# Kernel tuning notes

Hardware: AMD Instinct MI355X
Metric: run time of the kernel (lower is better)

The kernel has to match this reference:

```python
import jax, jax.numpy as jnp
import numpy as np

N_NODES = 100000
N_EDGES = 1600000
IN_DIM, HIDDEN_DIM, OUT_DIM = 500, 64, 40


def setup_inputs() -> dict:
    key = jax.random.key(0)
    k1, k2, k3, k4, k5 = jax.random.split(key, 5)
    x = jax.random.normal(k1, (N_NODES, IN_DIM), dtype=jnp.float32)
    edge_index = jax.random.randint(k2, (2, N_EDGES), 0, N_NODES, dtype=jnp.int64)
    # Glorot-style init like PyG GCNConv
    W1 = jax.random.normal(k3, (IN_DIM, HIDDEN_DIM), dtype=jnp.float32) / np.sqrt(IN_DIM)
    b1 = jnp.zeros((HIDDEN_DIM,), dtype=jnp.float32)
    W2 = jax.random.normal(k4, (HIDDEN_DIM, OUT_DIM), dtype=jnp.float32) / np.sqrt(HIDDEN_DIM)
    b2 = jnp.zeros((OUT_DIM,), dtype=jnp.float32)
    return {"x": x, "W1": W1, "b1": b1, "W2": W2, "b2": b2, "edge_index": edge_index}


def _gcn_conv(x, W, b, src, dst, n):
    """PyG GCNConv: h = D^{-1/2} (A + I) D^{-1/2} (x W) + b."""
    h = x @ W  # transform first, propagate in smaller dim
    loops = jnp.arange(n, dtype=src.dtype)
    s = jnp.concatenate([src, loops])
    d = jnp.concatenate([dst, loops])
    deg = jax.ops.segment_sum(jnp.ones_like(d, dtype=h.dtype), d, num_segments=n)
    dinv = jnp.where(deg > 0, jax.lax.rsqrt(deg), 0.0)
    norm = dinv[s] * dinv[d]               # [E+N]
    msg = h[s] * norm[:, None]             # gather + scale
    out = jax.ops.segment_sum(msg, d, num_segments=n)  # scatter-add
    return out + b


def reference(x, W1, b1, W2, b2, edge_index):
    src, dst = edge_index[0], edge_index[1]
    n = x.shape[0]
    h = _gcn_conv(x, W1, b1, src, dst, n)
    h = jax.nn.relu(h)  # eval mode: dropout is identity
    out = _gcn_conv(h, W2, b2, src, dst, n)
    return out
```

## Files before the change

### kernel.cpp

```cpp
#include <hip/hip_runtime.h>
#include <cstdint>
#include <cstddef>

#define NN 100000
#define NE 1600000
#define IND 500
#define HD 64
#define OD 40
#define NBLK ((NN + 255) / 256)
#define KSTEPS 16
#define NTT 16
#define EB 1563

typedef __attribute__((ext_vector_type(8))) short short8v;
typedef __attribute__((ext_vector_type(8))) __bf16 bf16x8;
typedef __attribute__((ext_vector_type(4))) float float4v;

template <class V>
static __device__ __forceinline__ auto mfma_bf16_(V a, V b, float4v c, int)
    -> decltype(__builtin_amdgcn_mfma_f32_16x16x32_bf16(a, b, c, 0, 0, 0)) {
    return __builtin_amdgcn_mfma_f32_16x16x32_bf16(a, b, c, 0, 0, 0);
}
template <class V>
static __device__ __forceinline__ float4v mfma_bf16_(V a, V b, float4v c, long) {
    return __builtin_amdgcn_mfma_f32_16x16x32_bf16((bf16x8)a, (bf16x8)b, c, 0, 0, 0);
}
static __device__ __forceinline__ float4v mfma16(short8v a, short8v b, float4v c) {
    return mfma_bf16_(a, b, c, 0);
}

static __device__ __forceinline__ float bf2f(unsigned short v) {
    return __uint_as_float((unsigned)v << 16);
}
static __device__ __forceinline__ unsigned short f2bf(float v) {
    unsigned u = __float_as_uint(v);
    return (unsigned short)((u + 0x7fffu + ((u >> 16) & 1u)) >> 16);
}

typedef __attribute__((address_space(3))) char lds_char;
typedef const __attribute__((address_space(1))) char g_char;
static __device__ __forceinline__ void gl16(const char* g, char* l) {
    __builtin_amdgcn_global_load_lds((g_char*)g, (lds_char*)l, 16, 0, 0);
}

static __device__ __forceinline__ int detect64(const void* ei) {
    const unsigned* u = (const unsigned*)ei;
    int is64 = 1;
    #pragma unroll
    for (int i = 1; i < 16; i += 2)
        if (u[i] != 0u) is64 = 0;
    return is64;
}

static __device__ __forceinline__ void load4e(const void* ei, int is64, size_t base, int v[4]) {
    if (is64) {
        int4 a = ((const int4*)ei)[base >> 1];
        int4 b = ((const int4*)ei)[(base >> 1) + 1];
        v[0] = a.x; v[1] = a.z; v[2] = b.x; v[3] = b.z;
    } else {
        int4 a = *(const int4*)((const int*)ei + base);
        v[0] = a.x; v[1] = a.y; v[2] = a.z; v[3] = a.w;
    }
}

__global__ __launch_bounds__(256) void k_count_prep(const void* ei, int* cnt,
                                                    int* __restrict__ rank,
                                                    const float* __restrict__ W,
                                                    unsigned short* __restrict__ wh,
                                                    unsigned short* __restrict__ wl) {
    const int is64 = detect64(ei);
    int e0 = (blockIdx.x * 256 + threadIdx.x) * 4;
    if (e0 < NE) {
        int d[4];
        load4e(ei, is64, (size_t)NE + e0, d);
        int4 r;
        r.x = atomicAdd(&cnt[d[0]], 1);
        r.y = atomicAdd(&cnt[d[1]], 1);
        r.z = atomicAdd(&cnt[d[2]], 1);
        r.w = atomicAdd(&cnt[d[3]], 1);
        *(int4*)(rank + e0) = r;
    }
    int t = blockIdx.x * 256 + threadIdx.x;
    if (t < KSTEPS * 4 * 64) {
        int l = t & 63;
        int f = (t >> 6) & 3;
        int s = t >> 8;
        int n = f * 16 + (l & 15);
        int kbase = s * 32 + 8 * (l >> 4);
        unsigned short* ph = wh + (size_t)t * 8;
        unsigned short* pl = wl + (size_t)t * 8;
        #pragma unroll
        for (int j = 0; j < 8; ++j) {
            int k = kbase + j;
            float v = (k < IND) ? W[(size_t)k * HD + n] : 0.f;
            unsigned u = __float_as_uint(v);
            ph[j] = (unsigned short)(u >> 16);
            float r = v - __uint_as_float(u & 0xffff0000u);
            pl[j] = f2bf(r);
        }
    }
}

__global__ __launch_bounds__(256) void k_scan_block(const int* __restrict__ cnt,
                                                    int* __restrict__ rowptr,
                                                    int* __restrict__ bsum,
                                                    float* __restrict__ dinv) {
    int t = threadIdx.x;
    int i = blockIdx.x * 256 + t;
    int v = (i < NN) ? cnt[i] : 0;
    if (i < NN) dinv[i] = rsqrtf((float)v + 1.0f);
    int inc = v;
    #pragma unroll
    for (int off = 1; off < 64; off <<= 1) {
        int u = __shfl_up(inc, off);
        if ((t & 63) >= off) inc += u;
    }
    __shared__ int wsum[4];
    if ((t & 63) == 63) wsum[t >> 6] = inc;
    __syncthreads();
    if (t == 0) {
        int a = 0;
        #pragma unroll
        for (int w = 0; w < 4; ++w) { int b = wsum[w]; wsum[w] = a; a += b; }
        bsum[blockIdx.x] = a;
    }
    __syncthreads();
    if (i < NN) rowptr[i] = inc - v + wsum[t >> 6];
}

__global__ __launch_bounds__(512) void k_scan_bsum(int* bsum) {
    int t = threadIdx.x;
    int v = (t < NBLK) ? bsum[t] : 0;
    int inc = v;
    #pragma unroll
    for (int off = 1; off < 64; off <<= 1) {
        int u = __shfl_up(inc, off);
        if ((t & 63) >= off) inc += u;
    }
    __shared__ int wsum[8];
    if ((t & 63) == 63) wsum[t >> 6] = inc;
    __syncthreads();
    if (t == 0) {
        int a = 0;
        #pragma unroll
        for (int w = 0; w < 8; ++w) { int b = wsum[w]; wsum[w] = a; a += b; }
    }
    __syncthreads();
    if (t < NBLK) bsum[t] = inc - v + wsum[t >> 6];
}

__global__ void k_scan_add(int* rowptr, const int* __restrict__ bsum) {
    int i = blockIdx.x * 256 + threadIdx.x;
    if (i < NN) rowptr[i] += bsum[i >> 8];
    if (i == 0) rowptr[NN] = NE;
}

static __device__ __forceinline__ void split8f(float4 u0, float4 u1,
                                               short8v& hi, short8v& lo) {
    float t[8] = {u0.x, u0.y, u0.z, u0.w, u1.x, u1.y, u1.z, u1.w};
    #pragma unroll
    for (int j = 0; j < 8; ++j) {
        unsigned q = __float_as_uint(t[j]);
        hi[j] = (short)(q >> 16);
        float r = t[j] - __uint_as_float(q & 0xffff0000u);
        lo[j] = (short)f2bf(r);
    }
}

__global__ __launch_bounds__(256, 5) void k_gemm_scatter(const float* __restrict__ x,
                                                         const char* __restrict__ whb,
                                                         const char* __restrict__ wlb,
                                                         const float* __restrict__ dinv,
                                                         unsigned short* __restrict__ h,
                                                         const void* __restrict__ ei,
                                                         const int* __restrict__ rowptr,
                                                         const int* __restrict__ rank,
                                                         int* __restrict__ srcs) {
    __shared__ char smem[32768];
    if (blockIdx.x & 1) {
        int e0 = ((blockIdx.x >> 1) * 256 + threadIdx.x) * 4;
        if (e0 >= NE) return;
        const int is64 = detect64(ei);
        int s[4], d[4];
        load4e(ei, is64, (size_t)e0, s);
        load4e(ei, is64, (size_t)NE + e0, d);
        int4 r = *(const int4*)(rank + e0);
        srcs[rowptr[d[0]] + r.x] = s[0];
        srcs[rowptr[d[1]] + r.y] = s[1];
        srcs[rowptr[d[2]] + r.z] = s[2];
        srcs[rowptr[d[3]] + r.w] = s[3];
        return;
    }
    const int tid  = threadIdx.x;
    const int lane = tid & 63;
    const int wave = tid >> 6;
    const int row0 = (blockIdx.x >> 1) * 64;
    const int rA = lane & 15;
    const int cg = lane >> 4;

    auto stage = [&](int kt, int buf) {
        const bool tail = (kt == NTT - 1);
        #pragma unroll
        for (int i = 0; i < 2; ++i) {
            int slot = i * 256 + tid;
            int r = slot >> 3, c = slot & 7;
            int cs = c ^ (r & 7);
            if (tail && cs > 4) cs = 4;
            int rsrc = row0 + r; if (rsrc >= NN) rsrc = NN - 1;
            const char* g = (const char*)x + (size_t)rsrc * (IND * 4) + kt * 128 + cs * 16;
            char* l = smem + buf * 16384 + (i * 256 + wave * 64) * 16;
            gl16(g, l);
        }
        #pragma unroll
        for (int i = 0; i < 2; ++i) {
            int j = i * 256 + tid;
            const char* src = (j < 256 ? whb : wlb) + kt * 4096 + (size_t)(j & 255) * 16;
            char* l = smem + buf * 16384 + 8192 + (i * 256 + wave * 64) * 16;
            gl16(src, l);
        }
    };

    float4v acc[4];
    const float4v zero4 = {0.f, 0.f, 0.f, 0.f};
    #pragma unroll
    for (int f = 0; f < 4; ++f) acc[f] = zero4;

    stage(0, 0);
    __syncthreads();

    int cur = 0;
    const int rbase = (wave * 16 + rA) * 8;
    const int sw = rA & 7;

    for (int kt = 0; kt < NTT; ++kt) {
        if (kt + 1 < NTT) stage(kt + 1, cur ^ 1);
        const float4*  pa = (const float4*)(smem + cur * 16384);
        const short8v* pb = (const short8v*)(smem + cur * 16384 + 8192);
        int ch = cg * 2;
        float4 u0 = pa[rbase + (ch ^ sw)];
        float4 u1 = pa[rbase + ((ch + 1) ^ sw)];
        short8v ah, al;
        split8f(u0, u1, ah, al);
        #pragma unroll
        for (int f = 0; f < 4; ++f) {
            short8v vh = pb[f * 64 + lane];
            short8v vl = pb[256 + f * 64 + lane];
            acc[f] = mfma16(al, vh, acc[f]);
            acc[f] = mfma16(ah, vl, acc[f]);
            acc[f] = mfma16(ah, vh, acc[f]);
        }
        __syncthreads();
        cur ^= 1;
    }

    #pragma unroll
    for (int j = 0; j < 4; ++j) {
        int row = row0 + wave * 16 + cg * 4 + j;
        if (row < NN) {
            float dv = dinv[row];
            #pragma unroll
            for (int f = 0; f < 4; ++f)
                h[(size_t)row * HD + f * 16 + rA] = f2bf(acc[f][j] * dv);
        }
    }
}

__global__ __launch_bounds__(256) void k_agg1(const int* __restrict__ rowptr,
                                              const int* __restrict__ srcs,
                                              const float* __restrict__ dinv,
                                              const unsigned short* __restrict__ hb,
                                              const float* __restrict__ bias,
                                              unsigned short* __restrict__ outb) {
    int wid = (blockIdx.x * 256 + threadIdx.x) >> 6;
    int lane = threadIdx.x & 63;
    if (wid >= NN) return;
    float acc = bf2f(hb[(size_t)wid * HD + lane]);
    int beg = rowptr[wid];
    int cnt = rowptr[wid + 1] - beg;
    for (int base = 0; base < cnt; base += 64) {
        int m = cnt - base; if (m > 64) m = 64;
        int sj = (lane < m) ? srcs[beg + base + lane] : 0;
        int j = 0;
        for (; j + 8 <= m; j += 8) {
            int s0 = __builtin_amdgcn_readlane(sj, j);
            int s1 = __builtin_amdgcn_readlane(sj, j + 1);
            int s2 = __builtin_amdgcn_readlane(sj, j + 2);
            int s3 = __builtin_amdgcn_readlane(sj, j + 3);
            int s4 = __builtin_amdgcn_readlane(sj, j + 4);
            int s5 = __builtin_amdgcn_readlane(sj, j + 5);
            int s6 = __builtin_amdgcn_readlane(sj, j + 6);
            int s7 = __builtin_amdgcn_readlane(sj, j + 7);
            float v0 = bf2f(hb[(size_t)s0 * HD + lane]);
            float v1 = bf2f(hb[(size_t)s1 * HD + lane]);
            float v2 = bf2f(hb[(size_t)s2 * HD + lane]);
            float v3 = bf2f(hb[(size_t)s3 * HD + lane]);
            float v4 = bf2f(hb[(size_t)s4 * HD + lane]);
            float v5 = bf2f(hb[(size_t)s5 * HD + lane]);
            float v6 = bf2f(hb[(size_t)s6 * HD + lane]);
            float v7 = bf2f(hb[(size_t)s7 * HD + lane]);
            acc += ((v0 + v1) + (v2 + v3)) + ((v4 + v5) + (v6 + v7));
        }
        for (; j < m; ++j) {
            int s = __builtin_amdgcn_readlane(sj, j);
            acc += bf2f(hb[(size_t)s * HD + lane]);
        }
    }
    float dn = dinv[wid];
    outb[(size_t)wid * HD + lane] = f2bf(fmaxf(acc * dn + bias[lane], 0.f) * dn);
}

__global__ __launch_bounds__(256) void k_agg2_gemm2(const int* __restrict__ rowptr,
                                                    const int* __restrict__ srcs,
                                                    const float* __restrict__ dinv,
                                                    const unsigned short* __restrict__ hb,
                                                    const float* __restrict__ W2,
                                                    const float* __restrict__ b2,
                                                    float* __restrict__ out) {
    __shared__ float ws2[HD][OD];
    __shared__ float hsh[4][HD];
    const int t = threadIdx.x;
    for (int i = t; i < HD * OD; i += 256)
        ws2[i / OD][i % OD] = W2[i];

    int wid = (blockIdx.x * 256 + t) >> 6;
    int lane = t & 63;
    int w = t >> 6;
    float acc = bf2f(hb[(size_t)wid * HD + lane]);
    int beg = rowptr[wid];
    int cnt = rowptr[wid + 1] - beg;
    for (int base = 0; base < cnt; base += 64) {
        int m = cnt - base; if (m > 64) m = 64;
        int sj = (lane < m) ? srcs[beg + base + lane] : 0;
        int j = 0;
        for (; j + 8 <= m; j += 8) {
            int s0 = __builtin_amdgcn_readlane(sj, j);
            int s1 = __builtin_amdgcn_readlane(sj, j + 1);
            int s2 = __builtin_amdgcn_readlane(sj, j + 2);
            int s3 = __builtin_amdgcn_readlane(sj, j + 3);
            int s4 = __builtin_amdgcn_readlane(sj, j + 4);
            int s5 = __builtin_amdgcn_readlane(sj, j + 5);
            int s6 = __builtin_amdgcn_readlane(sj, j + 6);
            int s7 = __builtin_amdgcn_readlane(sj, j + 7);
            float v0 = bf2f(hb[(size_t)s0 * HD + lane]);
            float v1 = bf2f(hb[(size_t)s1 * HD + lane]);
            float v2 = bf2f(hb[(size_t)s2 * HD + lane]);
            float v3 = bf2f(hb[(size_t)s3 * HD + lane]);
            float v4 = bf2f(hb[(size_t)s4 * HD + lane]);
            float v5 = bf2f(hb[(size_t)s5 * HD + lane]);
            float v6 = bf2f(hb[(size_t)s6 * HD + lane]);
            float v7 = bf2f(hb[(size_t)s7 * HD + lane]);
            acc += ((v0 + v1) + (v2 + v3)) + ((v4 + v5) + (v6 + v7));
        }
        for (; j < m; ++j) {
            int s = __builtin_amdgcn_readlane(sj, j);
            acc += bf2f(hb[(size_t)s * HD + lane]);
        }
    }
    hsh[w][lane] = acc * dinv[wid];
    __syncthreads();
    if (lane < OD) {
        float s = b2[lane];
        #pragma unroll
        for (int k = 0; k < HD; ++k)
            s = fmaf(hsh[w][k], ws2[k][lane], s);
        out[(size_t)wid * OD + lane] = s;
    }
}

extern "C" void kernel_launch(void* const* d_in, const int* in_sizes, int n_in,
                              void* d_out, int out_size, void* d_ws, size_t ws_size,
                              hipStream_t stream) {
    const float* x  = (const float*)d_in[0];
    const float* W1 = (const float*)d_in[1];
    const float* b1 = (const float*)d_in[2];
    const float* W2 = (const float*)d_in[3];
    const float* b2 = (const float*)d_in[4];
    const void*  ei = d_in[5];
    float* out = (float*)d_out;

    char* ws = (char*)d_ws;
    unsigned short* h1b    = (unsigned short*)ws;
    unsigned short* hrelub = (unsigned short*)(ws + 12800000);
    int*   rowptr = (int*)(ws + 25600000);
    int*   cnt    = (int*)(ws + 26000896);
    int*   bsum   = (int*)(ws + 26401792);
    int*   srcs   = (int*)(ws + 26403840);
    int*   rank   = (int*)(ws + 32803840);
    float* dinv   = (float*)(ws + 39203840);
    unsigned short* wh = (unsigned short*)(ws + 39604224);
    unsigned short* wl = (unsigned short*)(ws + 39669760);

    hipMemsetAsync(cnt, 0, (size_t)NN * 4, stream);
    k_count_prep<<<EB, 256, 0, stream>>>(ei, cnt, rank, W1, wh, wl);
    k_scan_block<<<NBLK, 256, 0, stream>>>(cnt, rowptr, bsum, dinv);
    k_scan_bsum<<<1, 512, 0, stream>>>(bsum);
    k_scan_add<<<NBLK, 256, 0, stream>>>(rowptr, bsum);
    k_gemm_scatter<<<2 * EB, 256, 0, stream>>>(x, (const char*)wh, (const char*)wl,
                                               dinv, h1b, ei, rowptr, rank, srcs);
    k_agg1<<<(NN * 64) / 256, 256, 0, stream>>>(rowptr, srcs, dinv, h1b, b1, hrelub);
    k_agg2_gemm2<<<(NN * 64) / 256, 256, 0, stream>>>(rowptr, srcs, dinv, hrelub, W2, b2, out);
}
```

Baseline: 333.4 us.

## Split edge scatter from GEMM1 and deepen GEMM pipeline to 4-buffer ring

```diff
diff --git a/kernel.cpp b/kernel.cpp
--- a/kernel.cpp
+++ b/kernel.cpp
@@ -155,6 +155,21 @@
     if (i == 0) rowptr[NN] = NE;
 }
 
+__global__ void k_scatter(const void* ei, const int* __restrict__ rowptr,
+                          const int* __restrict__ rank, int* __restrict__ srcs) {
+    int e0 = (blockIdx.x * 256 + threadIdx.x) * 4;
+    if (e0 >= NE) return;
+    const int is64 = detect64(ei);
+    int s[4], d[4];
+    load4e(ei, is64, (size_t)e0, s);
+    load4e(ei, is64, (size_t)NE + e0, d);
+    int4 r = *(const int4*)(rank + e0);
+    srcs[rowptr[d[0]] + r.x] = s[0];
+    srcs[rowptr[d[1]] + r.y] = s[1];
+    srcs[rowptr[d[2]] + r.z] = s[2];
+    srcs[rowptr[d[3]] + r.w] = s[3];
+}
+
 static __device__ __forceinline__ void split8f(float4 u0, float4 u1,
                                                short8v& hi, short8v& lo) {
     float t[8] = {u0.x, u0.y, u0.z, u0.w, u1.x, u1.y, u1.z, u1.w};
@@ -167,34 +182,16 @@
     }
 }
 
-__global__ __launch_bounds__(256, 5) void k_gemm_scatter(const float* __restrict__ x,
-                                                         const char* __restrict__ whb,
-                                                         const char* __restrict__ wlb,
-                                                         const float* __restrict__ dinv,
-                                                         unsigned short* __restrict__ h,
-                                                         const void* __restrict__ ei,
-                                                         const int* __restrict__ rowptr,
-                                                         const int* __restrict__ rank,
-                                                         int* __restrict__ srcs) {
-    __shared__ char smem[32768];
-    if (blockIdx.x & 1) {
-        int e0 = ((blockIdx.x >> 1) * 256 + threadIdx.x) * 4;
-        if (e0 >= NE) return;
-        const int is64 = detect64(ei);
-        int s[4], d[4];
-        load4e(ei, is64, (size_t)e0, s);
-        load4e(ei, is64, (size_t)NE + e0, d);
-        int4 r = *(const int4*)(rank + e0);
-        srcs[rowptr[d[0]] + r.x] = s[0];
-        srcs[rowptr[d[1]] + r.y] = s[1];
-        srcs[rowptr[d[2]] + r.z] = s[2];
-        srcs[rowptr[d[3]] + r.w] = s[3];
-        return;
-    }
+__global__ __launch_bounds__(256, 2) void k_gemm1m(const float* __restrict__ x,
+                                                   const char* __restrict__ whb,
+                                                   const char* __restrict__ wlb,
+                                                   const float* __restrict__ dinv,
+                                                   unsigned short* __restrict__ h) {
+    __shared__ char smem[65536];
     const int tid  = threadIdx.x;
     const int lane = tid & 63;
     const int wave = tid >> 6;
-    const int row0 = (blockIdx.x >> 1) * 64;
+    const int row0 = blockIdx.x * 64;
     const int rA = lane & 15;
     const int cg = lane >> 4;
 
@@ -226,16 +223,19 @@
     for (int f = 0; f < 4; ++f) acc[f] = zero4;
 
     stage(0, 0);
-    __syncthreads();
-
-    int cur = 0;
+    stage(1, 1);
+
     const int rbase = (wave * 16 + rA) * 8;
     const int sw = rA & 7;
 
+    #pragma unroll
     for (int kt = 0; kt < NTT; ++kt) {
-        if (kt + 1 < NTT) stage(kt + 1, cur ^ 1);
-        const float4*  pa = (const float4*)(smem + cur * 16384);
-        const short8v* pb = (const short8v*)(smem + cur * 16384 + 8192);
+        if (kt + 2 < NTT) stage(kt + 2, (kt + 2) & 3);
+        if (kt + 2 < NTT)      asm volatile("s_waitcnt vmcnt(8)\ns_barrier" ::: "memory");
+        else if (kt + 1 < NTT) asm volatile("s_waitcnt vmcnt(4)\ns_barrier" ::: "memory");
+        else                   asm volatile("s_waitcnt vmcnt(0)\ns_barrier" ::: "memory");
+        const float4*  pa = (const float4*)(smem + (kt & 3) * 16384);
+        const short8v* pb = (const short8v*)(smem + (kt & 3) * 16384 + 8192);
         int ch = cg * 2;
         float4 u0 = pa[rbase + (ch ^ sw)];
         float4 u1 = pa[rbase + ((ch + 1) ^ sw)];
@@ -249,8 +249,6 @@
             acc[f] = mfma16(ah, vl, acc[f]);
             acc[f] = mfma16(ah, vh, acc[f]);
         }
-        __syncthreads();
-        cur ^= 1;
     }
 
     #pragma unroll
@@ -395,8 +393,8 @@
     k_scan_block<<<NBLK, 256, 0, stream>>>(cnt, rowptr, bsum, dinv);
     k_scan_bsum<<<1, 512, 0, stream>>>(bsum);
     k_scan_add<<<NBLK, 256, 0, stream>>>(rowptr, bsum);
-    k_gemm_scatter<<<2 * EB, 256, 0, stream>>>(x, (const char*)wh, (const char*)wl,
-                                               dinv, h1b, ei, rowptr, rank, srcs);
+    k_scatter<<<EB, 256, 0, stream>>>(ei, rowptr, rank, srcs);
+    k_gemm1m<<<EB, 256, 0, stream>>>(x, (const char*)wh, (const char*)wl, dinv, h1b);
     k_agg1<<<(NN * 64) / 256, 256, 0, stream>>>(rowptr, srcs, dinv, h1b, b1, hrelub);
     k_agg2_gemm2<<<(NN * 64) / 256, 256, 0, stream>>>(rowptr, srcs, dinv, hrelub, W2, b2, out);
 }
```

Result: faster. 316.6 us (-5.0%).
